# Kernel tuning notes

Hardware: AMD Instinct MI355X
Metric: run time of the kernel (lower is better)

## Reference

```python
import jax, jax.numpy as jnp
import numpy as np

B, M, E, D, NCAT = 8, 4096, 1024, 128, 64


def setup_inputs() -> dict:
    key = jax.random.key(0)
    ks = jax.random.split(key, 9)
    node_feats = jax.random.normal(ks[0], (B, M, D), dtype=jnp.float32)
    inc_mat = (jax.random.uniform(ks[1], (B, M, E)) < 0.05).astype(jnp.float32)
    s = 1.0 / np.sqrt(D)
    W_att = jax.random.uniform(ks[2], (D, D), minval=-s, maxval=s)      # VertexConv.attention (no bias)
    W_proj = jax.random.uniform(ks[3], (D, D), minval=-s, maxval=s)     # VertexConv.projection (no bias)
    ec_att_w = jax.random.uniform(ks[4], (1, D), minval=-s, maxval=s)   # EdgeAggregation.attention (no bias)
    ec_proj_w = jax.random.uniform(ks[5], (D, D), minval=-s, maxval=s)  # EdgeAggregation.projection
    ec_proj_b = jax.random.uniform(ks[6], (D,), minval=-s, maxval=s)
    fc_w = jax.random.uniform(ks[7], (NCAT, D), minval=-s, maxval=s)
    fc_b = jax.random.uniform(ks[8], (NCAT,), minval=-s, maxval=s)
    return {"node_feats": node_feats, "inc_mat": inc_mat, "W_att": W_att,
            "W_proj": W_proj, "ec_att_w": ec_att_w, "ec_proj_w": ec_proj_w,
            "ec_proj_b": ec_proj_b, "fc_w": fc_w, "fc_b": fc_b}


def reference(node_feats, inc_mat, W_att, W_proj, ec_att_w, ec_proj_w, ec_proj_b, fc_w, fc_b):
    # ---- VertexConv: node -> edge aggregation with per-channel attention over edges ----
    node_scores = jnp.einsum('bmd,kd->bmk', node_feats, W_att)          # (b,m,d)
    edge_scores = jnp.einsum('bme,bmd->bed', inc_mat, node_scores)      # inc^T @ scores
    attn = jax.nn.softmax(edge_scores, axis=1)                          # softmax over edge dim
    # original: einsum('bme,bmd->bmed') then contract m with attn; equivalent to:
    agg = jnp.einsum('bme,bmd->bed', inc_mat, node_feats)               # (b,e,d)
    edge_feat = (agg * attn) @ W_proj.T                                 # (b,e,d)
    # ---- HypergraphEdgeAggregation: attention-pool over edges ----
    a = edge_feat @ ec_att_w.T                                          # (b,e,1)
    w = jax.nn.softmax(a, axis=1)
    pooled = jnp.sum(edge_feat * w, axis=1)                             # (b,d)
    out = pooled @ ec_proj_w.T + ec_proj_b                              # (b,d)
    logits = out @ fc_w.T + fc_b                                        # (b,ncat)
    return logits
```

## Files before the change

### kernel.cpp

```cpp
#include <hip/hip_runtime.h>

#define BB 8
#define MM 4096
#define EE 1024
#define DD 128
#define NCAT 64

typedef __attribute__((ext_vector_type(8))) short bf16x8;
typedef __attribute__((ext_vector_type(4))) float f32x4;

__global__ __launch_bounds__(256, 1) void k_magg(const float* __restrict__ nf,
                                                 const float* __restrict__ inc,
                                                 float* __restrict__ part) {
    int bid = blockIdx.x;
    int b  = bid & 7;
    int et = (bid >> 3) & 7;
    int ks = bid >> 6;

    __shared__ ushort As2[4][128][8];
    __shared__ ushort Bh2[4][128][8];
    __shared__ ushort Bl2[4][128][8];

    int tid  = threadIdx.x;
    int lane = tid & 63;
    int w    = tid >> 6;
    int we   = (w & 1) * 64;
    int wd   = (w >> 1) * 64;

    int ecol = tid & 127;
    int mh   = tid >> 7;

    long m0base = (long)ks * 1024;
    const float* incc = inc + ((long)b * MM + m0base + mh * 16) * EE + (et * 128 + ecol);
    const float* nfc  = nf  + ((long)b * MM + m0base + mh * 16) * DD + ecol;

    f32x4 acc[4][4];
#pragma unroll
    for (int i = 0; i < 4; ++i)
#pragma unroll
        for (int j = 0; j < 4; ++j) acc[i][j] = (f32x4)(0.0f);

#define LOADM(ra, rb, t)                                                      \
    do {                                                                      \
        _Pragma("unroll")                                                     \
        for (int j2 = 0; j2 < 16; ++j2) {                                     \
            ra[j2] = incc[(long)((t) * 32 + j2) * EE];                        \
            rb[j2] = nfc[(long)((t) * 32 + j2) * DD];                         \
        }                                                                     \
    } while (0)

#define STOREM(ra, rb)                                                        \
    do {                                                                      \
        uint ua[8], uh[8], ul[8];                                             \
        _Pragma("unroll")                                                     \
        for (int q = 0; q < 8; ++q) {                                         \
            ua[q] = (__float_as_uint(ra[2 * q]) >> 16) |                      \
                    (__float_as_uint(ra[2 * q + 1]) & 0xffff0000u);           \
            float x0 = rb[2 * q], x1 = rb[2 * q + 1];                         \
            uint h0 = __float_as_uint(x0) & 0xffff0000u;                      \
            uint h1 = __float_as_uint(x1) & 0xffff0000u;                      \
            uh[q] = (h0 >> 16) | h1;                                          \
            float l0 = x0 - __uint_as_float(h0);                              \
            float l1 = x1 - __uint_as_float(h1);                              \
            ul[q] = (__float_as_uint(l0) >> 16) |                             \
                    (__float_as_uint(l1) & 0xffff0000u);                      \
        }                                                                     \
        *(uint4*)&As2[2 * mh][ecol][0]     = make_uint4(ua[0], ua[1], ua[2], ua[3]); \
        *(uint4*)&As2[2 * mh + 1][ecol][0] = make_uint4(ua[4], ua[5], ua[6], ua[7]); \
        *(uint4*)&Bh2[2 * mh][ecol][0]     = make_uint4(uh[0], uh[1], uh[2], uh[3]); \
        *(uint4*)&Bh2[2 * mh + 1][ecol][0] = make_uint4(uh[4], uh[5], uh[6], uh[7]); \
        *(uint4*)&Bl2[2 * mh][ecol][0]     = make_uint4(ul[0], ul[1], ul[2], ul[3]); \
        *(uint4*)&Bl2[2 * mh + 1][ecol][0] = make_uint4(ul[4], ul[5], ul[6], ul[7]); \
    } while (0)

#define COMPUTEM()                                                            \
    do {                                                                      \
        int kg = lane >> 4, rr = lane & 15;                                   \
        bf16x8 af[4];                                                         \
        _Pragma("unroll")                                                     \
        for (int i = 0; i < 4; ++i)                                           \
            af[i] = *(const bf16x8*)&As2[kg][we + i * 16 + rr][0];            \
        _Pragma("unroll")                                                     \
        for (int j = 0; j < 4; ++j) {                                         \
            bf16x8 bh = *(const bf16x8*)&Bh2[kg][wd + j * 16 + rr][0];        \
            bf16x8 bl = *(const bf16x8*)&Bl2[kg][wd + j * 16 + rr][0];        \
            _Pragma("unroll")                                                 \
            for (int i = 0; i < 4; ++i) {                                     \
                acc[i][j] = __builtin_amdgcn_mfma_f32_16x16x32_bf16(af[i], bh, acc[i][j], 0, 0, 0); \
                acc[i][j] = __builtin_amdgcn_mfma_f32_16x16x32_bf16(af[i], bl, acc[i][j], 0, 0, 0); \
            }                                                                 \
        }                                                                     \
    } while (0)

    float a0[16], b0[16], a1[16], b1[16];
    LOADM(a0, b0, 0);
    LOADM(a1, b1, 1);
    const int NT = 32;
    for (int t = 0; t < NT; t += 2) {
        STOREM(a0, b0);
        __syncthreads();
        if (t + 2 < NT) LOADM(a0, b0, t + 2);
        COMPUTEM();
        __syncthreads();
        STOREM(a1, b1);
        __syncthreads();
        if (t + 3 < NT) LOADM(a1, b1, t + 3);
        COMPUTEM();
        __syncthreads();
    }

    float* pp = part + (long)ks * ((long)BB * EE * DD) + ((long)b * EE + et * 128) * DD;
#pragma unroll
    for (int i = 0; i < 4; ++i)
#pragma unroll
        for (int j = 0; j < 4; ++j) {
            int e = we + i * 16 + ((lane >> 4) << 2);
            int d = wd + j * 16 + (lane & 15);
#pragma unroll
            for (int r = 0; r < 4; ++r)
                pp[(long)(e + r) * DD + d] = acc[i][j][r];
        }
#undef LOADM
#undef STOREM
#undef COMPUTEM
}

__global__ __launch_bounds__(256) void k_score(const float* __restrict__ part,
                                               float* __restrict__ agg,
                                               const float* __restrict__ W,
                                               float* __restrict__ Y) {
    __shared__ float Wt[128][129];
    __shared__ float xt[16][128];
    int tid = threadIdx.x;
    for (int t = tid; t < 128 * 128; t += 256) Wt[t & 127][t >> 7] = W[t];
    long r0 = (long)blockIdx.x * 16;
    const long PS = (long)BB * EE * DD;
    for (int t = tid; t < 2048; t += 256) {
        long off = r0 * 128 + t;
        float v = part[off] + part[off + PS] + part[off + 2 * PS] + part[off + 3 * PS];
        xt[t >> 7][t & 127] = v;
        agg[off] = v;
    }
    __syncthreads();
    int j = tid & 127, half = tid >> 7;
    float acc[8] = {0, 0, 0, 0, 0, 0, 0, 0};
    for (int k = 0; k < 128; k += 4) {
        float w0 = Wt[k][j], w1 = Wt[k + 1][j], w2 = Wt[k + 2][j], w3 = Wt[k + 3][j];
#pragma unroll
        for (int el = 0; el < 8; ++el) {
            float4 x4 = *(const float4*)&xt[half * 8 + el][k];
            acc[el] += x4.x * w0; acc[el] += x4.y * w1;
            acc[el] += x4.z * w2; acc[el] += x4.w * w3;
        }
    }
#pragma unroll
    for (int el = 0; el < 8; ++el) Y[(r0 + half * 8 + el) * 128 + j] = acc[el];
}

__global__ __launch_bounds__(256) void k_colsum(const float* __restrict__ S,
                                                float* __restrict__ colsum) {
    int b = blockIdx.x & 7, ch = blockIdx.x >> 3;
    int d = threadIdx.x & 127, eh = threadIdx.x >> 7;
    const float* Sb = S + ((long)b * EE + ch * 64) * DD + d;
    float s = 0.0f;
    for (int e = eh; e < 64; e += 2) s += __expf(Sb[(long)e * DD]);
    atomicAdd(&colsum[b * DD + d], s);
}

__global__ __launch_bounds__(256) void k_proj(const float* __restrict__ S,
                                              const float* __restrict__ agg,
                                              const float* __restrict__ colsum,
                                              const float* __restrict__ W,
                                              float* __restrict__ Y,
                                              const float* __restrict__ att,
                                              float* __restrict__ abuf,
                                              float* __restrict__ sumA) {
    __shared__ float Wt[128][129];
    __shared__ float xt[16][128];
    __shared__ float ared[4][8];
    __shared__ float aex[16];
    int tid = threadIdx.x;
    for (int t = tid; t < 128 * 128; t += 256) Wt[t & 127][t >> 7] = W[t];
    long r0 = (long)blockIdx.x * 16;
    int b = (int)(r0 >> 10);
    float rinv = 1.0f / colsum[b * DD + (tid & 127)];
    for (int t = tid; t < 2048; t += 256) {
        long off = r0 * 128 + t;
        xt[t >> 7][t & 127] = __expf(S[off]) * rinv * agg[off];
    }
    __syncthreads();
    int j = tid & 127, half = tid >> 7;
    float acc[8] = {0, 0, 0, 0, 0, 0, 0, 0};
    for (int k = 0; k < 128; k += 4) {
        float w0 = Wt[k][j], w1 = Wt[k + 1][j], w2 = Wt[k + 2][j], w3 = Wt[k + 3][j];
#pragma unroll
        for (int el = 0; el < 8; ++el) {
            float4 x4 = *(const float4*)&xt[half * 8 + el][k];
            acc[el] += x4.x * w0; acc[el] += x4.y * w1;
            acc[el] += x4.z * w2; acc[el] += x4.w * w3;
        }
    }
#pragma unroll
    for (int el = 0; el < 8; ++el) Y[(r0 + half * 8 + el) * 128 + j] = acc[el];
    float av = att[j];
    float contrib[8];
#pragma unroll
    for (int el = 0; el < 8; ++el) contrib[el] = acc[el] * av;
#pragma unroll
    for (int off2 = 32; off2 > 0; off2 >>= 1)
#pragma unroll
        for (int el = 0; el < 8; ++el) contrib[el] += __shfl_xor(contrib[el], off2, 64);
    int lane = tid & 63, wv = tid >> 6;
    if (lane == 0)
#pragma unroll
        for (int el = 0; el < 8; ++el) ared[wv][el] = contrib[el];
    __syncthreads();
    if (tid < 16) {
        int hh = tid >> 3, el = tid & 7;
        float a = ared[hh * 2][el] + ared[hh * 2 + 1][el];
        float ea = __expf(a);
        abuf[r0 + tid] = ea;
        aex[tid] = ea;
    }
    __syncthreads();
    if (tid == 0) {
        float s2 = 0.0f;
#pragma unroll
        for (int i = 0; i < 16; ++i) s2 += aex[i];
        atomicAdd(&sumA[b], s2);
    }
}

__global__ __launch_bounds__(256) void k_pool(const float* __restrict__ ef,
                                              const float* __restrict__ abuf,
                                              float* __restrict__ praw) {
    int b = blockIdx.x & 7, ch = blockIdx.x >> 3;
    int d = threadIdx.x & 127, eh = threadIdx.x >> 7;
    const float* efb = ef + ((long)b * EE + ch * 64) * DD + d;
    const float* ab = abuf + b * EE + ch * 64;
    float s = 0.0f;
    for (int e = eh; e < 64; e += 2) s += ab[e] * efb[(long)e * DD];
    atomicAdd(&praw[b * DD + d], s);
}

__global__ __launch_bounds__(128) void k_out(const float* __restrict__ praw,
                                             const float* __restrict__ sumA,
                                             const float* __restrict__ ec_pw,
                                             const float* __restrict__ ec_pb,
                                             const float* __restrict__ fc_w,
                                             const float* __restrict__ fc_b,
                                             float* __restrict__ out) {
    int b = blockIdx.x, tid = threadIdx.x;
    __shared__ float pooled[DD];
    __shared__ float outv[DD];
    float rinv = 1.0f / sumA[b];
    pooled[tid] = praw[b * DD + tid] * rinv;
    __syncthreads();
    float o = ec_pb[tid];
    const float* wr = ec_pw + tid * DD;
    for (int k = 0; k < DD; ++k) o += pooled[k] * wr[k];
    outv[tid] = o;
    __syncthreads();
    if (tid < NCAT) {
        float o2 = fc_b[tid];
        const float* wr2 = fc_w + tid * DD;
        for (int k = 0; k < DD; ++k) o2 += outv[k] * wr2[k];
        out[b * NCAT + tid] = o2;
    }
}

extern "C" void kernel_launch(void* const* d_in, const int* in_sizes, int n_in,
                              void* d_out, int out_size, void* d_ws, size_t ws_size,
                              hipStream_t stream) {
    const float* nf     = (const float*)d_in[0];
    const float* inc    = (const float*)d_in[1];
    const float* W_att  = (const float*)d_in[2];
    const float* W_proj = (const float*)d_in[3];
    const float* ec_att = (const float*)d_in[4];
    const float* ec_pw  = (const float*)d_in[5];
    const float* ec_pb  = (const float*)d_in[6];
    const float* fc_w   = (const float*)d_in[7];
    const float* fc_b   = (const float*)d_in[8];
    float* out = (float*)d_out;

    const long PS = (long)BB * EE * DD;
    char* ws = (char*)d_ws;
    float* part   = (float*)ws;
    float* agg    = (float*)(ws + 4 * PS * 4);
    float* sc     = agg + PS;
    float* stats  = sc + PS;
    float* colsum = stats;
    float* praw   = stats + 1024;
    float* sumA   = stats + 2048;
    float* abuf   = stats + 2056;
    float* ef     = part;

    hipMemsetAsync(stats, 0, (2048 + 8) * sizeof(float), stream);
    k_magg<<<256, 256, 0, stream>>>(nf, inc, part);
    k_score<<<(BB * EE) / 16, 256, 0, stream>>>(part, agg, W_att, sc);
    k_colsum<<<BB * 16, 256, 0, stream>>>(sc, colsum);
    k_proj<<<(BB * EE) / 16, 256, 0, stream>>>(sc, agg, colsum, W_proj, ef, ec_att, abuf, sumA);
    k_pool<<<BB * 16, 256, 0, stream>>>(ef, abuf, praw);
    k_out<<<BB, 128, 0, stream>>>(praw, sumA, ec_pw, ec_pb, fc_w, fc_b, out);
}
```

Measured before the change: 282.5 us.

## Retile incidence GEMM to 64-edge tiles and fuse colsum and pooling into neighbours

```diff
diff --git a/kernel.cpp b/kernel.cpp
--- a/kernel.cpp
+++ b/kernel.cpp
@@ -9,109 +9,103 @@
 typedef __attribute__((ext_vector_type(8))) short bf16x8;
 typedef __attribute__((ext_vector_type(4))) float f32x4;
 
-__global__ __launch_bounds__(256, 1) void k_magg(const float* __restrict__ nf,
+__device__ __forceinline__ unsigned pk(float lo, float hi) {
+    return __builtin_amdgcn_perm(__float_as_uint(hi), __float_as_uint(lo), 0x07060302u);
+}
+
+__global__ __launch_bounds__(256, 2) void k_magg(const float* __restrict__ nf,
                                                  const float* __restrict__ inc,
                                                  float* __restrict__ part) {
     int bid = blockIdx.x;
     int b  = bid & 7;
-    int et = (bid >> 3) & 7;
-    int ks = bid >> 6;
-
-    __shared__ ushort As2[4][128][8];
-    __shared__ ushort Bh2[4][128][8];
-    __shared__ ushort Bl2[4][128][8];
+    int et = (bid >> 3) & 15;
+    int ks = bid >> 7;
+
+    __shared__ __align__(16) unsigned short As[4][64][8];
+    __shared__ __align__(16) unsigned short Bh[4][128][8];
+    __shared__ __align__(16) unsigned short Bl[4][128][8];
 
     int tid  = threadIdx.x;
     int lane = tid & 63;
     int w    = tid >> 6;
-    int we   = (w & 1) * 64;
+    int we   = (w & 1) * 32;
     int wd   = (w >> 1) * 64;
 
-    int ecol = tid & 127;
-    int mh   = tid >> 7;
-
-    long m0base = (long)ks * 1024;
-    const float* incc = inc + ((long)b * MM + m0base + mh * 16) * EE + (et * 128 + ecol);
-    const float* nfc  = nf  + ((long)b * MM + m0base + mh * 16) * DD + ecol;
-
-    f32x4 acc[4][4];
-#pragma unroll
-    for (int i = 0; i < 4; ++i)
+    int ecolA = tid & 63;
+    int mgrpA = tid >> 6;
+    int dcolB = tid & 127;
+    int mhB   = tid >> 7;
+
+    long m0 = (long)ks * 1024;
+    const float* incp = inc + ((long)b * MM + m0) * EE + et * 64 + ecolA;
+    const float* nfp  = nf  + ((long)b * MM + m0) * DD + dcolB;
+
+    f32x4 acc[2][4];
+#pragma unroll
+    for (int i = 0; i < 2; ++i)
 #pragma unroll
         for (int j = 0; j < 4; ++j) acc[i][j] = (f32x4)(0.0f);
 
-#define LOADM(ra, rb, t)                                                      \
-    do {                                                                      \
-        _Pragma("unroll")                                                     \
-        for (int j2 = 0; j2 < 16; ++j2) {                                     \
-            ra[j2] = incc[(long)((t) * 32 + j2) * EE];                        \
-            rb[j2] = nfc[(long)((t) * 32 + j2) * DD];                         \
-        }                                                                     \
-    } while (0)
-
-#define STOREM(ra, rb)                                                        \
-    do {                                                                      \
-        uint ua[8], uh[8], ul[8];                                             \
-        _Pragma("unroll")                                                     \
-        for (int q = 0; q < 8; ++q) {                                         \
-            ua[q] = (__float_as_uint(ra[2 * q]) >> 16) |                      \
-                    (__float_as_uint(ra[2 * q + 1]) & 0xffff0000u);           \
-            float x0 = rb[2 * q], x1 = rb[2 * q + 1];                         \
-            uint h0 = __float_as_uint(x0) & 0xffff0000u;                      \
-            uint h1 = __float_as_uint(x1) & 0xffff0000u;                      \
-            uh[q] = (h0 >> 16) | h1;                                          \
-            float l0 = x0 - __uint_as_float(h0);                              \
-            float l1 = x1 - __uint_as_float(h1);                              \
-            ul[q] = (__float_as_uint(l0) >> 16) |                             \
-                    (__float_as_uint(l1) & 0xffff0000u);                      \
-        }                                                                     \
-        *(uint4*)&As2[2 * mh][ecol][0]     = make_uint4(ua[0], ua[1], ua[2], ua[3]); \
-        *(uint4*)&As2[2 * mh + 1][ecol][0] = make_uint4(ua[4], ua[5], ua[6], ua[7]); \
-        *(uint4*)&Bh2[2 * mh][ecol][0]     = make_uint4(uh[0], uh[1], uh[2], uh[3]); \
-        *(uint4*)&Bh2[2 * mh + 1][ecol][0] = make_uint4(uh[4], uh[5], uh[6], uh[7]); \
-        *(uint4*)&Bl2[2 * mh][ecol][0]     = make_uint4(ul[0], ul[1], ul[2], ul[3]); \
-        *(uint4*)&Bl2[2 * mh + 1][ecol][0] = make_uint4(ul[4], ul[5], ul[6], ul[7]); \
-    } while (0)
-
-#define COMPUTEM()                                                            \
-    do {                                                                      \
-        int kg = lane >> 4, rr = lane & 15;                                   \
-        bf16x8 af[4];                                                         \
-        _Pragma("unroll")                                                     \
-        for (int i = 0; i < 4; ++i)                                           \
-            af[i] = *(const bf16x8*)&As2[kg][we + i * 16 + rr][0];            \
-        _Pragma("unroll")                                                     \
-        for (int j = 0; j < 4; ++j) {                                         \
-            bf16x8 bh = *(const bf16x8*)&Bh2[kg][wd + j * 16 + rr][0];        \
-            bf16x8 bl = *(const bf16x8*)&Bl2[kg][wd + j * 16 + rr][0];        \
-            _Pragma("unroll")                                                 \
-            for (int i = 0; i < 4; ++i) {                                     \
-                acc[i][j] = __builtin_amdgcn_mfma_f32_16x16x32_bf16(af[i], bh, acc[i][j], 0, 0, 0); \
-                acc[i][j] = __builtin_amdgcn_mfma_f32_16x16x32_bf16(af[i], bl, acc[i][j], 0, 0, 0); \
-            }                                                                 \
-        }                                                                     \
-    } while (0)
-
-    float a0[16], b0[16], a1[16], b1[16];
-    LOADM(a0, b0, 0);
-    LOADM(a1, b1, 1);
-    const int NT = 32;
-    for (int t = 0; t < NT; t += 2) {
-        STOREM(a0, b0);
+    float ra[8], rb[16];
+
+#define LOADM(t) do {                                                         \
+    _Pragma("unroll")                                                         \
+    for (int j2 = 0; j2 < 8; ++j2)                                            \
+        ra[j2] = incp[(long)((t) * 32 + mgrpA * 8 + j2) * EE];                \
+    _Pragma("unroll")                                                         \
+    for (int j2 = 0; j2 < 16; ++j2)                                           \
+        rb[j2] = nfp[(long)((t) * 32 + mhB * 16 + j2) * DD];                  \
+} while (0)
+
+#define STOREM() do {                                                         \
+    unsigned ua[4];                                                           \
+    _Pragma("unroll")                                                         \
+    for (int q = 0; q < 4; ++q) ua[q] = pk(ra[2 * q], ra[2 * q + 1]);         \
+    *(uint4*)&As[mgrpA][ecolA][0] = make_uint4(ua[0], ua[1], ua[2], ua[3]);   \
+    unsigned uh[8], ul[8];                                                    \
+    _Pragma("unroll")                                                         \
+    for (int q = 0; q < 8; ++q) {                                             \
+        float x0 = rb[2 * q], x1 = rb[2 * q + 1];                             \
+        uh[q] = pk(x0, x1);                                                   \
+        float h0 = __uint_as_float(__float_as_uint(x0) & 0xffff0000u);        \
+        float h1 = __uint_as_float(__float_as_uint(x1) & 0xffff0000u);        \
+        ul[q] = pk(x0 - h0, x1 - h1);                                         \
+    }                                                                         \
+    *(uint4*)&Bh[2 * mhB][dcolB][0]     = make_uint4(uh[0], uh[1], uh[2], uh[3]); \
+    *(uint4*)&Bh[2 * mhB + 1][dcolB][0] = make_uint4(uh[4], uh[5], uh[6], uh[7]); \
+    *(uint4*)&Bl[2 * mhB][dcolB][0]     = make_uint4(ul[0], ul[1], ul[2], ul[3]); \
+    *(uint4*)&Bl[2 * mhB + 1][dcolB][0] = make_uint4(ul[4], ul[5], ul[6], ul[7]); \
+} while (0)
+
+    LOADM(0);
+    for (int t = 0; t < 32; ++t) {
+        STOREM();
+        if (t + 1 < 32) LOADM(t + 1);
         __syncthreads();
-        if (t + 2 < NT) LOADM(a0, b0, t + 2);
-        COMPUTEM();
+        {
+            int kg = lane >> 4, rr = lane & 15;
+            bf16x8 af[2];
+#pragma unroll
+            for (int i = 0; i < 2; ++i)
+                af[i] = *(const bf16x8*)&As[kg][we + i * 16 + rr][0];
+#pragma unroll
+            for (int j = 0; j < 4; ++j) {
+                bf16x8 bh = *(const bf16x8*)&Bh[kg][wd + j * 16 + rr][0];
+                bf16x8 bl = *(const bf16x8*)&Bl[kg][wd + j * 16 + rr][0];
+#pragma unroll
+                for (int i = 0; i < 2; ++i) {
+                    acc[i][j] = __builtin_amdgcn_mfma_f32_16x16x32_bf16(af[i], bh, acc[i][j], 0, 0, 0);
+                    acc[i][j] = __builtin_amdgcn_mfma_f32_16x16x32_bf16(af[i], bl, acc[i][j], 0, 0, 0);
+                }
+            }
+        }
         __syncthreads();
-        STOREM(a1, b1);
-        __syncthreads();
-        if (t + 3 < NT) LOADM(a1, b1, t + 3);
-        COMPUTEM();
-        __syncthreads();
-    }
-
-    float* pp = part + (long)ks * ((long)BB * EE * DD) + ((long)b * EE + et * 128) * DD;
-#pragma unroll
-    for (int i = 0; i < 4; ++i)
+    }
+
+    const long PS = (long)BB * EE * DD;
+    float* pp = part + (long)ks * PS + ((long)b * EE + et * 64) * DD;
+#pragma unroll
+    for (int i = 0; i < 2; ++i)
 #pragma unroll
         for (int j = 0; j < 4; ++j) {
             int e = we + i * 16 + ((lane >> 4) << 2);
@@ -122,15 +116,16 @@
         }
 #undef LOADM
 #undef STOREM
-#undef COMPUTEM
 }
 
 __global__ __launch_bounds__(256) void k_score(const float* __restrict__ part,
                                                float* __restrict__ agg,
                                                const float* __restrict__ W,
-                                               float* __restrict__ Y) {
+                                               float* __restrict__ esc,
+                                               float* __restrict__ colsum) {
     __shared__ float Wt[128][129];
     __shared__ float xt[16][128];
+    __shared__ float cred[2][128];
     int tid = threadIdx.x;
     for (int t = tid; t < 128 * 128; t += 256) Wt[t & 127][t >> 7] = W[t];
     long r0 = (long)blockIdx.x * 16;
@@ -153,32 +148,33 @@
             acc[el] += x4.z * w2; acc[el] += x4.w * w3;
         }
     }
-#pragma unroll
-    for (int el = 0; el < 8; ++el) Y[(r0 + half * 8 + el) * 128 + j] = acc[el];
-}
-
-__global__ __launch_bounds__(256) void k_colsum(const float* __restrict__ S,
-                                                float* __restrict__ colsum) {
-    int b = blockIdx.x & 7, ch = blockIdx.x >> 3;
-    int d = threadIdx.x & 127, eh = threadIdx.x >> 7;
-    const float* Sb = S + ((long)b * EE + ch * 64) * DD + d;
-    float s = 0.0f;
-    for (int e = eh; e < 64; e += 2) s += __expf(Sb[(long)e * DD]);
-    atomicAdd(&colsum[b * DD + d], s);
-}
-
-__global__ __launch_bounds__(256) void k_proj(const float* __restrict__ S,
+    float csum = 0.0f;
+#pragma unroll
+    for (int el = 0; el < 8; ++el) {
+        float es = __expf(acc[el]);
+        esc[(r0 + half * 8 + el) * 128 + j] = es;
+        csum += es;
+    }
+    cred[half][j] = csum;
+    __syncthreads();
+    if (half == 0) {
+        int b = (int)(r0 >> 10);
+        atomicAdd(&colsum[b * DD + j], cred[0][j] + cred[1][j]);
+    }
+}
+
+__global__ __launch_bounds__(256) void k_proj(const float* __restrict__ esc,
                                               const float* __restrict__ agg,
                                               const float* __restrict__ colsum,
                                               const float* __restrict__ W,
-                                              float* __restrict__ Y,
                                               const float* __restrict__ att,
-                                              float* __restrict__ abuf,
+                                              float* __restrict__ praw,
                                               float* __restrict__ sumA) {
     __shared__ float Wt[128][129];
     __shared__ float xt[16][128];
     __shared__ float ared[4][8];
     __shared__ float aex[16];
+    __shared__ float pred[2][128];
     int tid = threadIdx.x;
     for (int t = tid; t < 128 * 128; t += 256) Wt[t & 127][t >> 7] = W[t];
     long r0 = (long)blockIdx.x * 16;
@@ -186,7 +182,7 @@
     float rinv = 1.0f / colsum[b * DD + (tid & 127)];
     for (int t = tid; t < 2048; t += 256) {
         long off = r0 * 128 + t;
-        xt[t >> 7][t & 127] = __expf(S[off]) * rinv * agg[off];
+        xt[t >> 7][t & 127] = esc[off] * rinv * agg[off];
     }
     __syncthreads();
     int j = tid & 127, half = tid >> 7;
@@ -200,8 +196,6 @@
             acc[el] += x4.z * w2; acc[el] += x4.w * w3;
         }
     }
-#pragma unroll
-    for (int el = 0; el < 8; ++el) Y[(r0 + half * 8 + el) * 128 + j] = acc[el];
     float av = att[j];
     float contrib[8];
 #pragma unroll
@@ -209,7 +203,8 @@
 #pragma unroll
     for (int off2 = 32; off2 > 0; off2 >>= 1)
 #pragma unroll
-        for (int el = 0; el < 8; ++el) contrib[el] += __shfl_xor(contrib[el], off2, 64);
+        for (int el = 0; el < 8; ++el)
+            contrib[el] += __shfl_xor(contrib[el], off2, 64);
     int lane = tid & 63, wv = tid >> 6;
     if (lane == 0)
 #pragma unroll
@@ -217,30 +212,21 @@
     __syncthreads();
     if (tid < 16) {
         int hh = tid >> 3, el = tid & 7;
-        float a = ared[hh * 2][el] + ared[hh * 2 + 1][el];
-        float ea = __expf(a);
-        abuf[r0 + tid] = ea;
-        aex[tid] = ea;
+        aex[tid] = __expf(ared[hh * 2][el] + ared[hh * 2 + 1][el]);
     }
     __syncthreads();
     if (tid == 0) {
-        float s2 = 0.0f;
-#pragma unroll
-        for (int i = 0; i < 16; ++i) s2 += aex[i];
-        atomicAdd(&sumA[b], s2);
-    }
-}
-
-__global__ __launch_bounds__(256) void k_pool(const float* __restrict__ ef,
-                                              const float* __restrict__ abuf,
-                                              float* __restrict__ praw) {
-    int b = blockIdx.x & 7, ch = blockIdx.x >> 3;
-    int d = threadIdx.x & 127, eh = threadIdx.x >> 7;
-    const float* efb = ef + ((long)b * EE + ch * 64) * DD + d;
-    const float* ab = abuf + b * EE + ch * 64;
-    float s = 0.0f;
-    for (int e = eh; e < 64; e += 2) s += ab[e] * efb[(long)e * DD];
-    atomicAdd(&praw[b * DD + d], s);
+        float s = 0.0f;
+#pragma unroll
+        for (int i = 0; i < 16; ++i) s += aex[i];
+        atomicAdd(&sumA[b], s);
+    }
+    float p = 0.0f;
+#pragma unroll
+    for (int el = 0; el < 8; ++el) p += aex[half * 8 + el] * acc[el];
+    pred[half][j] = p;
+    __syncthreads();
+    if (half == 0) atomicAdd(&praw[b * DD + j], pred[0][j] + pred[1][j]);
 }
 
 __global__ __launch_bounds__(128) void k_out(const float* __restrict__ praw,
@@ -287,19 +273,15 @@
     char* ws = (char*)d_ws;
     float* part   = (float*)ws;
     float* agg    = (float*)(ws + 4 * PS * 4);
-    float* sc     = agg + PS;
-    float* stats  = sc + PS;
+    float* esc    = agg + PS;
+    float* stats  = esc + PS;
     float* colsum = stats;
     float* praw   = stats + 1024;
     float* sumA   = stats + 2048;
-    float* abuf   = stats + 2056;
-    float* ef     = part;
 
     hipMemsetAsync(stats, 0, (2048 + 8) * sizeof(float), stream);
-    k_magg<<<256, 256, 0, stream>>>(nf, inc, part);
-    k_score<<<(BB * EE) / 16, 256, 0, stream>>>(part, agg, W_att, sc);
-    k_colsum<<<BB * 16, 256, 0, stream>>>(sc, colsum);
-    k_proj<<<(BB * EE) / 16, 256, 0, stream>>>(sc, agg, colsum, W_proj, ef, ec_att, abuf, sumA);
-    k_pool<<<BB * 16, 256, 0, stream>>>(ef, abuf, praw);
+    k_magg<<<512, 256, 0, stream>>>(nf, inc, part);
+    k_score<<<(BB * EE) / 16, 256, 0, stream>>>(part, agg, W_att, esc, colsum);
+    k_proj<<<(BB * EE) / 16, 256, 0, stream>>>(esc, agg, colsum, W_proj, ec_att, praw, sumA);
     k_out<<<BB, 128, 0, stream>>>(praw, sumA, ec_pw, ec_pb, fc_w, fc_b, out);
 }
```

New measurement: 265.1 us. 6.2% less time.
